# Optimization experiments

Hardware: AMD Instinct MI355X
Metric: run time of the kernel (lower is better)

The kernel has to match this reference:

```python
import jax, jax.numpy as jnp
import numpy as np
from jax import lax

H = 64            # hidden size
NUM_LAYERS = 3
EMBED_LEN = 128
B, T = 256, 2048


def _lstm_layer(x, Wih, Whh, bih, bhh):
    """x: [B, T, in]; returns full hidden sequence [B, T, H].
    PyTorch gate order: i, f, g, o."""
    Bn = x.shape[0]
    b = bih + bhh  # [4H]
    # Precompute input contribution for all timesteps: [T, B, 4H]
    xg = jnp.einsum('bti,gi->tbg', x, Wih) + b
    h0 = jnp.zeros((Bn, H), x.dtype)
    c0 = jnp.zeros((Bn, H), x.dtype)

    def step(carry, xg_t):
        h, c = carry
        gates = xg_t + h @ Whh.T  # [B, 4H]
        i, f, g, o = jnp.split(gates, 4, axis=-1)
        i = jax.nn.sigmoid(i)
        f = jax.nn.sigmoid(f)
        g = jnp.tanh(g)
        o = jax.nn.sigmoid(o)
        c = f * c + i * g
        h = o * jnp.tanh(c)
        return (h, c), h

    (_, _), hs = lax.scan(step, (h0, c0), xg)  # hs: [T, B, H]
    return jnp.swapaxes(hs, 0, 1)              # [B, T, H]


def setup_inputs() -> dict:
    key = jax.random.key(0)
    ks = jax.random.split(key, 20)
    k = 1.0 / np.sqrt(H)  # PyTorch default init bound

    def u(kk, shape):
        return jax.random.uniform(kk, shape, jnp.float32, -k, k)

    inp = {"x": jax.random.normal(ks[0], (B, 1, T), jnp.float32)}
    in_sizes = [1, H, H]
    idx = 1
    for l in range(NUM_LAYERS):
        inp[f"Wih{l}"] = u(ks[idx], (4 * H, in_sizes[l])); idx += 1
        inp[f"Whh{l}"] = u(ks[idx], (4 * H, H)); idx += 1
        inp[f"bih{l}"] = u(ks[idx], (4 * H,)); idx += 1
        inp[f"bhh{l}"] = u(ks[idx], (4 * H,)); idx += 1
    inp["fcW"] = u(ks[idx], (EMBED_LEN, H)); idx += 1
    inp["fcb"] = u(ks[idx], (EMBED_LEN,))
    return inp


def reference(x, Wih0, Whh0, bih0, bhh0,
              Wih1, Whh1, bih1, bhh1,
              Wih2, Whh2, bih2, bhh2,
              fcW, fcb):
    # forward: transpose [B,1,T] -> [B,T,1]
    h = jnp.swapaxes(x, 1, 2)
    h = _lstm_layer(h, Wih0, Whh0, bih0, bhh0)
    h = _lstm_layer(h, Wih1, Whh1, bih1, bhh1)
    h = _lstm_layer(h, Wih2, Whh2, bih2, bhh2)
    last = h[:, -1, :]              # [B, H]
    return last @ fcW.T + fcb       # [B, EMBED_LEN]
```

## Files before the change

kernel.cpp:

```cpp
#include <hip/hip_runtime.h>

#define T_LEN 2048
#define HID 64
#define EMB 128
#define WD 8
#define NWIN (T_LEN / WD)
#define NPH (NWIN + 4)
#define PPAD (HID + 4)

typedef _Float16 half2_t __attribute__((ext_vector_type(2)));
typedef _Float16 half4 __attribute__((ext_vector_type(4)));
typedef _Float16 half8 __attribute__((ext_vector_type(8)));
typedef float f32x4 __attribute__((ext_vector_type(4)));
typedef unsigned uint4v __attribute__((ext_vector_type(4)));

#if __has_builtin(__builtin_amdgcn_exp2f)
#define EXP2F(x) __builtin_amdgcn_exp2f(x)
#else
#define EXP2F(x) exp2f(x)
#endif
#if __has_builtin(__builtin_amdgcn_rcpf)
#define RCPF(x) __builtin_amdgcn_rcpf(x)
#else
#define RCPF(x) (1.0f / (x))
#endif

#define LOG2E 1.4426950408889634f

__device__ __forceinline__ float fdot2(unsigned a, unsigned b, float c) {
    return __builtin_amdgcn_fdot2(__builtin_bit_cast(half2_t, a),
                                  __builtin_bit_cast(half2_t, b), c, false);
}

__device__ __forceinline__ float dotrow(const uint4v* w, const uint4v* g, float init) {
    float a0 = init, a1 = 0.f, a2 = 0.f, a3 = 0.f;
    #pragma unroll
    for (int q = 0; q < 8; ++q) {
        a0 = fdot2(w[q][0], g[q][0], a0);
        a1 = fdot2(w[q][1], g[q][1], a1);
        a2 = fdot2(w[q][2], g[q][2], a2);
        a3 = fdot2(w[q][3], g[q][3], a3);
    }
    return (a0 + a1) + (a2 + a3);
}

__device__ __forceinline__ uint4v pack8(float4 a, float4 b, float s) {
    half2_t h0{(_Float16)(a.x * s), (_Float16)(a.y * s)};
    half2_t h1{(_Float16)(a.z * s), (_Float16)(a.w * s)};
    half2_t h2{(_Float16)(b.x * s), (_Float16)(b.y * s)};
    half2_t h3{(_Float16)(b.z * s), (_Float16)(b.w * s)};
    uint4v q;
    q[0] = __builtin_bit_cast(unsigned, h0);
    q[1] = __builtin_bit_cast(unsigned, h1);
    q[2] = __builtin_bit_cast(unsigned, h2);
    q[3] = __builtin_bit_cast(unsigned, h3);
    return q;
}

__device__ __forceinline__ void cvt8(const float* __restrict__ Wp, float s, uint4v* dst) {
    const float4* p = reinterpret_cast<const float4*>(Wp);
    #pragma unroll
    for (int k = 0; k < 8; ++k) dst[k] = pack8(p[2 * k], p[2 * k + 1], s);
}

__global__ __launch_bounds__(512)
__attribute__((amdgpu_waves_per_eu(2, 2)))
void lstm3_fused(
    const float* __restrict__ x,
    const float* __restrict__ Wih0, const float* __restrict__ Whh0,
    const float* __restrict__ bih0, const float* __restrict__ bhh0,
    const float* __restrict__ Wih1, const float* __restrict__ Whh1,
    const float* __restrict__ bih1, const float* __restrict__ bhh1,
    const float* __restrict__ Wih2, const float* __restrict__ Whh2,
    const float* __restrict__ bih2, const float* __restrict__ bhh2,
    const float* __restrict__ fcW,  const float* __restrict__ fcb,
    float* __restrict__ out)
{
    const int b   = blockIdx.x;
    const int tid = threadIdx.x;
    const int wv  = tid >> 6;
    const int L   = tid & 63;

    __shared__ __align__(16) _Float16 h0ring[16][HID];
    __shared__ __align__(16) _Float16 h1ring[16][HID];
    __shared__ __align__(16) _Float16 h2ring[2][HID];
    __shared__ __align__(16) float p1buf[2][WD][4][PPAD];
    __shared__ __align__(16) float p2buf[2][WD][4][PPAD];
    __shared__ __align__(16) float xs[T_LEN];

    {
        const float4* xg4 = reinterpret_cast<const float4*>(x + b * T_LEN);
        reinterpret_cast<float4*>(xs)[tid] = xg4[tid];
        reinterpret_cast<unsigned*>(h0ring)[tid] = 0u;
        reinterpret_cast<unsigned*>(h1ring)[tid] = 0u;
        if (tid < 64) reinterpret_cast<unsigned*>(h2ring)[tid] = 0u;
    }

    const float sI = -LOG2E, sF = -LOG2E, sG = -2.f * LOG2E, sO = -LOG2E;
    const float scl[4] = {sI, sF, sG, sO};

    uint4v w[4][8];
    float bias4[4] = {0.f, 0.f, 0.f, 0.f};
    float wx4[4]   = {0.f, 0.f, 0.f, 0.f};

    if (wv < 3) {
        const float* Wh = (wv == 0) ? Whh0 : (wv == 1) ? Whh1 : Whh2;
        const float* bi = (wv == 0) ? bih0 : (wv == 1) ? bih1 : bih2;
        const float* bh = (wv == 0) ? bhh0 : (wv == 1) ? bhh1 : bhh2;
        #pragma unroll
        for (int c = 0; c < 4; ++c) {
            cvt8(Wh + (c * 64 + L) * 64, scl[c], w[c]);
            bias4[c] = (bi[c * 64 + L] + bh[c * 64 + L]) * scl[c];
        }
        if (wv == 0) {
            #pragma unroll
            for (int c = 0; c < 4; ++c) wx4[c] = Wih0[c * 64 + L] * scl[c];
        }
    } else if (wv == 3 || wv == 7) {
        const float* Wsrc = (wv == 3) ? Wih1 : Wih2;
        const int g4 = (L >> 4) * 4;
        const int mr = L & 15;
        #pragma unroll
        for (int t = 0; t < 16; ++t) {
            const float s = scl[t >> 2];
            const float* rowp = Wsrc + (t * 16 + mr) * 64;
            #pragma unroll
            for (int kf = 0; kf < 2; ++kf) {
                float4 lo = *reinterpret_cast<const float4*>(rowp + kf * 32 + g4);
                float4 hi = *reinterpret_cast<const float4*>(rowp + kf * 32 + 16 + g4);
                half8 a = {(_Float16)(lo.x * s), (_Float16)(lo.y * s),
                           (_Float16)(lo.z * s), (_Float16)(lo.w * s),
                           (_Float16)(hi.x * s), (_Float16)(hi.y * s),
                           (_Float16)(hi.z * s), (_Float16)(hi.w * s)};
                const int idx = t * 2 + kf;
                w[idx >> 3][idx & 7] = __builtin_bit_cast(uint4v, a);
            }
        }
    }

    float cst = 0.f;
    __syncthreads();

    for (int ph = 0; ph < NPH; ++ph) {
        const int par = ph & 1;

        if (wv == 0) {
            if (ph < NWIN) {
                _Float16* cur = &h0ring[par * 8][0];
                const _Float16* prv = &h0ring[(par ^ 1) * 8][0];
                const int tb = ph * WD;
                #pragma unroll
                for (int j = 0; j < WD; ++j) {
                    const uint4v* hp = reinterpret_cast<const uint4v*>(
                        (j == 0) ? (prv + 7 * HID) : (cur + (j - 1) * HID));
                    uint4v g[8];
                    #pragma unroll
                    for (int k = 0; k < 8; ++k) g[k] = hp[k];
                    float xv = xs[tb + j];
                    float d0 = dotrow(w[0], g, fmaf(wx4[0], xv, bias4[0]));
                    float d1 = dotrow(w[1], g, fmaf(wx4[1], xv, bias4[1]));
                    float d2 = dotrow(w[2], g, fmaf(wx4[2], xv, bias4[2]));
                    float d3 = dotrow(w[3], g, fmaf(wx4[3], xv, bias4[3]));
                    float ai = RCPF(1.f + EXP2F(d0));
                    float af = RCPF(1.f + EXP2F(d1));
                    float ag = fmaf(2.f, RCPF(1.f + EXP2F(d2)), -1.f);
                    float ao = RCPF(1.f + EXP2F(d3));
                    cst = fmaf(af, cst, ai * ag);
                    float tc = fmaf(2.f, RCPF(1.f + EXP2F(-2.f * LOG2E * cst)), -1.f);
                    cur[j * HID + L] = (_Float16)(ao * tc);
                }
            }
        } else if (wv == 1) {
            if (ph >= 2 && ph < NWIN + 2) {
                _Float16* cur = &h1ring[par * 8][0];
                const _Float16* prv = &h1ring[(par ^ 1) * 8][0];
                const float (*pb)[4][PPAD] = p1buf[par];
                #pragma unroll
                for (int j = 0; j < WD; ++j) {
                    const uint4v* hp = reinterpret_cast<const uint4v*>(
                        (j == 0) ? (prv + 7 * HID) : (cur + (j - 1) * HID));
                    uint4v g[8];
                    #pragma unroll
                    for (int k = 0; k < 8; ++k) g[k] = hp[k];
                    float d0 = dotrow(w[0], g, bias4[0] + pb[j][0][L]);
                    float d1 = dotrow(w[1], g, bias4[1] + pb[j][1][L]);
                    float d2 = dotrow(w[2], g, bias4[2] + pb[j][2][L]);
                    float d3 = dotrow(w[3], g, bias4[3] + pb[j][3][L]);
                    float ai = RCPF(1.f + EXP2F(d0));
                    float af = RCPF(1.f + EXP2F(d1));
                    float ag = fmaf(2.f, RCPF(1.f + EXP2F(d2)), -1.f);
                    float ao = RCPF(1.f + EXP2F(d3));
                    cst = fmaf(af, cst, ai * ag);
                    float tc = fmaf(2.f, RCPF(1.f + EXP2F(-2.f * LOG2E * cst)), -1.f);
                    cur[j * HID + L] = (_Float16)(ao * tc);
                }
            }
        } else if (wv == 2) {
            if (ph >= 4) {
                const float (*pb)[4][PPAD] = p2buf[par];
                #pragma unroll
                for (int j = 0; j < WD; ++j) {
                    const uint4v* hp = reinterpret_cast<const uint4v*>(
                        &h2ring[(j & 1) ^ 1][0]);
                    uint4v g[8];
                    #pragma unroll
                    for (int k = 0; k < 8; ++k) g[k] = hp[k];
                    float d0 = dotrow(w[0], g, bias4[0] + pb[j][0][L]);
                    float d1 = dotrow(w[1], g, bias4[1] + pb[j][1][L]);
                    float d2 = dotrow(w[2], g, bias4[2] + pb[j][2][L]);
                    float d3 = dotrow(w[3], g, bias4[3] + pb[j][3][L]);
                    float ai = RCPF(1.f + EXP2F(d0));
                    float af = RCPF(1.f + EXP2F(d1));
                    float ag = fmaf(2.f, RCPF(1.f + EXP2F(d2)), -1.f);
                    float ao = RCPF(1.f + EXP2F(d3));
                    cst = fmaf(af, cst, ai * ag);
                    float tc = fmaf(2.f, RCPF(1.f + EXP2F(-2.f * LOG2E * cst)), -1.f);
                    h2ring[j & 1][L] = (_Float16)(ao * tc);
                }
            }
        } else if (wv == 3 || wv == 7) {
            const bool act = (wv == 3) ? (ph >= 1 && ph < NWIN + 1)
                                       : (ph >= 3 && ph < NWIN + 3);
            if (act) {
                const _Float16 (*ring)[HID] = (wv == 3) ? h0ring : h1ring;
                float (*po)[4][PPAD] = ((wv == 3) ? p1buf : p2buf)[par ^ 1];
                const int jj = L & 7;
                const int g4 = (L >> 4) * 4;
                const _Float16* rb = &ring[(par ^ 1) * 8 + jj][0];
                half4 b00 = *reinterpret_cast<const half4*>(rb + g4);
                half4 b01 = *reinterpret_cast<const half4*>(rb + 16 + g4);
                half4 b10 = *reinterpret_cast<const half4*>(rb + 32 + g4);
                half4 b11 = *reinterpret_cast<const half4*>(rb + 48 + g4);
                half8 B0 = __builtin_shufflevector(b00, b01, 0, 1, 2, 3, 4, 5, 6, 7);
                half8 B1 = __builtin_shufflevector(b10, b11, 0, 1, 2, 3, 4, 5, 6, 7);
                f32x4 acc[16];
                #pragma unroll
                for (int t = 0; t < 16; ++t) {
                    const int i0 = t * 2, i1 = t * 2 + 1;
                    f32x4 z = {0.f, 0.f, 0.f, 0.f};
                    acc[t] = __builtin_amdgcn_mfma_f32_16x16x32_f16(
                        __builtin_bit_cast(half8, w[i0 >> 3][i0 & 7]), B0, z, 0, 0, 0);
                    acc[t] = __builtin_amdgcn_mfma_f32_16x16x32_f16(
                        __builtin_bit_cast(half8, w[i1 >> 3][i1 & 7]), B1, acc[t], 0, 0, 0);
                }
                if ((L & 15) < 8) {
                    #pragma unroll
                    for (int t = 0; t < 16; ++t) {
                        *reinterpret_cast<f32x4*>(
                            &po[jj][t >> 2][(t & 3) * 16 + g4]) = acc[t];
                    }
                }
            }
        }

        __syncthreads();
    }

    if (tid < EMB) {
        float acc = fcb[tid];
        const _Float16* hf = &h2ring[1][0];
        const float4* W4 = reinterpret_cast<const float4*>(fcW + tid * HID);
        #pragma unroll
        for (int k = 0; k < 16; ++k) {
            float4 wv4 = W4[k];
            acc = fmaf(wv4.x, (float)hf[4 * k + 0], acc);
            acc = fmaf(wv4.y, (float)hf[4 * k + 1], acc);
            acc = fmaf(wv4.z, (float)hf[4 * k + 2], acc);
            acc = fmaf(wv4.w, (float)hf[4 * k + 3], acc);
        }
        out[b * EMB + tid] = acc;
    }
}

extern "C" void kernel_launch(void* const* d_in, const int* in_sizes, int n_in,
                              void* d_out, int out_size, void* d_ws, size_t ws_size,
                              hipStream_t stream) {
    const float* x    = (const float*)d_in[0];
    const float* Wih0 = (const float*)d_in[1];
    const float* Whh0 = (const float*)d_in[2];
    const float* bih0 = (const float*)d_in[3];
    const float* bhh0 = (const float*)d_in[4];
    const float* Wih1 = (const float*)d_in[5];
    const float* Whh1 = (const float*)d_in[6];
    const float* bih1 = (const float*)d_in[7];
    const float* bhh1 = (const float*)d_in[8];
    const float* Wih2 = (const float*)d_in[9];
    const float* Whh2 = (const float*)d_in[10];
    const float* bih2 = (const float*)d_in[11];
    const float* bhh2 = (const float*)d_in[12];
    const float* fcW  = (const float*)d_in[13];
    const float* fcb  = (const float*)d_in[14];
    float* out = (float*)d_out;

    lstm3_fused<<<dim3(256), dim3(512), 0, stream>>>(
        x, Wih0, Whh0, bih0, bhh0,
        Wih1, Whh1, bih1, bhh1,
        Wih2, Whh2, bih2, bhh2,
        fcW, fcb, out);
}
```

Before: 1.021 ms.

## Pipeline LSTM layers across blocks with MFMA batching over 32 samples

Replaces the one-block-per-sample kernel, where waves handled the three layers of a single sequence, with 24 blocks: 8 sample groups by 3 layers. Each block runs 32 samples at once and computes the recurrent gates with MFMA over the batch dimension. Hidden states stream between layer blocks through a global-memory ring buffer, coordinated by acquire/release flag spinning. This trades a large per-sample serial dot-product cost for batched tensor-core work. The risks are that only 24 CUs are used, inter-block flag latency sits on every step, and the design relies on all 24 blocks being co-resident to avoid deadlock.

```diff
diff --git a/kernel.cpp b/kernel.cpp
--- a/kernel.cpp
+++ b/kernel.cpp
@@ -3,16 +3,14 @@
 #define T_LEN 2048
 #define HID 64
 #define EMB 128
-#define WD 8
-#define NWIN (T_LEN / WD)
-#define NPH (NWIN + 4)
-#define PPAD (HID + 4)
-
-typedef _Float16 half2_t __attribute__((ext_vector_type(2)));
-typedef _Float16 half4 __attribute__((ext_vector_type(4)));
-typedef _Float16 half8 __attribute__((ext_vector_type(8)));
+#define NGRP 8
+#define SPG 32
+#define RSLOT 64
+#define HPAD 68
+
+typedef _Float16 half4v __attribute__((ext_vector_type(4)));
+typedef _Float16 half8v __attribute__((ext_vector_type(8)));
 typedef float f32x4 __attribute__((ext_vector_type(4)));
-typedef unsigned uint4v __attribute__((ext_vector_type(4)));
 
 #if __has_builtin(__builtin_amdgcn_exp2f)
 #define EXP2F(x) __builtin_amdgcn_exp2f(x)
@@ -27,45 +25,25 @@
 
 #define LOG2E 1.4426950408889634f
 
-__device__ __forceinline__ float fdot2(unsigned a, unsigned b, float c) {
-    return __builtin_amdgcn_fdot2(__builtin_bit_cast(half2_t, a),
-                                  __builtin_bit_cast(half2_t, b), c, false);
-}
-
-__device__ __forceinline__ float dotrow(const uint4v* w, const uint4v* g, float init) {
-    float a0 = init, a1 = 0.f, a2 = 0.f, a3 = 0.f;
-    #pragma unroll
-    for (int q = 0; q < 8; ++q) {
-        a0 = fdot2(w[q][0], g[q][0], a0);
-        a1 = fdot2(w[q][1], g[q][1], a1);
-        a2 = fdot2(w[q][2], g[q][2], a2);
-        a3 = fdot2(w[q][3], g[q][3], a3);
-    }
-    return (a0 + a1) + (a2 + a3);
-}
-
-__device__ __forceinline__ uint4v pack8(float4 a, float4 b, float s) {
-    half2_t h0{(_Float16)(a.x * s), (_Float16)(a.y * s)};
-    half2_t h1{(_Float16)(a.z * s), (_Float16)(a.w * s)};
-    half2_t h2{(_Float16)(b.x * s), (_Float16)(b.y * s)};
-    half2_t h3{(_Float16)(b.z * s), (_Float16)(b.w * s)};
-    uint4v q;
-    q[0] = __builtin_bit_cast(unsigned, h0);
-    q[1] = __builtin_bit_cast(unsigned, h1);
-    q[2] = __builtin_bit_cast(unsigned, h2);
-    q[3] = __builtin_bit_cast(unsigned, h3);
-    return q;
-}
-
-__device__ __forceinline__ void cvt8(const float* __restrict__ Wp, float s, uint4v* dst) {
-    const float4* p = reinterpret_cast<const float4*>(Wp);
-    #pragma unroll
-    for (int k = 0; k < 8; ++k) dst[k] = pack8(p[2 * k], p[2 * k + 1], s);
+__device__ __forceinline__ half8v ldA(const float* __restrict__ rowp, int kbase,
+                                      int g4, float s) {
+    float4 lo = *reinterpret_cast<const float4*>(rowp + kbase + g4);
+    float4 hi = *reinterpret_cast<const float4*>(rowp + kbase + 16 + g4);
+    half8v a = {(_Float16)(lo.x * s), (_Float16)(lo.y * s),
+                (_Float16)(lo.z * s), (_Float16)(lo.w * s),
+                (_Float16)(hi.x * s), (_Float16)(hi.y * s),
+                (_Float16)(hi.z * s), (_Float16)(hi.w * s)};
+    return a;
+}
+
+__device__ __forceinline__ half8v ldB(const _Float16* base, int kbase, int g4) {
+    half4v lo = *reinterpret_cast<const half4v*>(base + kbase + g4);
+    half4v hi = *reinterpret_cast<const half4v*>(base + kbase + 16 + g4);
+    return __builtin_shufflevector(lo, hi, 0, 1, 2, 3, 4, 5, 6, 7);
 }
 
 __global__ __launch_bounds__(512)
-__attribute__((amdgpu_waves_per_eu(2, 2)))
-void lstm3_fused(
+void lstm3_pipe(
     const float* __restrict__ x,
     const float* __restrict__ Wih0, const float* __restrict__ Whh0,
     const float* __restrict__ bih0, const float* __restrict__ bhh0,
@@ -74,201 +52,185 @@
     const float* __restrict__ Wih2, const float* __restrict__ Whh2,
     const float* __restrict__ bih2, const float* __restrict__ bhh2,
     const float* __restrict__ fcW,  const float* __restrict__ fcb,
-    float* __restrict__ out)
+    float* __restrict__ out, char* __restrict__ ws)
 {
-    const int b   = blockIdx.x;
+    const int bid = blockIdx.x;
+    const int lay = bid >> 3;
+    const int grp = bid & 7;
     const int tid = threadIdx.x;
     const int wv  = tid >> 6;
+    const int qd  = wv >> 2;
+    const int q   = wv & 3;
     const int L   = tid & 63;
-
-    __shared__ __align__(16) _Float16 h0ring[16][HID];
-    __shared__ __align__(16) _Float16 h1ring[16][HID];
-    __shared__ __align__(16) _Float16 h2ring[2][HID];
-    __shared__ __align__(16) float p1buf[2][WD][4][PPAD];
-    __shared__ __align__(16) float p2buf[2][WD][4][PPAD];
-    __shared__ __align__(16) float xs[T_LEN];
-
-    {
-        const float4* xg4 = reinterpret_cast<const float4*>(x + b * T_LEN);
-        reinterpret_cast<float4*>(xs)[tid] = xg4[tid];
-        reinterpret_cast<unsigned*>(h0ring)[tid] = 0u;
-        reinterpret_cast<unsigned*>(h1ring)[tid] = 0u;
-        if (tid < 64) reinterpret_cast<unsigned*>(h2ring)[tid] = 0u;
-    }
+    const int mr  = L & 15;
+    const int lg  = L >> 4;
+    const int g4  = 4 * lg;
+    const int sl  = 16 * qd + mr;
+    const int sample = SPG * grp + sl;
+
+    __shared__ __align__(16) _Float16 hbuf[2][SPG][HPAD];
+
+    int* flags = (int*)ws;
+    int* prod0 = flags + grp;
+    int* cons0 = flags + 8 + grp;
+    int* prod1 = flags + 16 + grp;
+    int* cons1 = flags + 24 + grp;
+    int* pf_in  = (lay == 2) ? prod1 : prod0;
+    int* cf_pub = (lay == 2) ? cons1 : cons0;
+    int* pf_pub = (lay == 0) ? prod0 : prod1;
+    int* cf_thr = (lay == 0) ? cons0 : cons1;
+
+    const size_t STREAM_ELEMS = (size_t)NGRP * RSLOT * SPG * HID;
+    _Float16* st0 = (_Float16*)(ws + 1024);
+    _Float16* st1 = st0 + STREAM_ELEMS;
+    const _Float16* stin = (lay == 2) ? st1 : st0;
+    _Float16*      stout = (lay == 0) ? st0 : st1;
+
+    for (int i = tid; i < 2176; i += 512)
+        reinterpret_cast<unsigned*>(hbuf)[i] = 0u;
 
     const float sI = -LOG2E, sF = -LOG2E, sG = -2.f * LOG2E, sO = -LOG2E;
     const float scl[4] = {sI, sF, sG, sO};
-
-    uint4v w[4][8];
-    float bias4[4] = {0.f, 0.f, 0.f, 0.f};
-    float wx4[4]   = {0.f, 0.f, 0.f, 0.f};
-
-    if (wv < 3) {
-        const float* Wh = (wv == 0) ? Whh0 : (wv == 1) ? Whh1 : Whh2;
-        const float* bi = (wv == 0) ? bih0 : (wv == 1) ? bih1 : bih2;
-        const float* bh = (wv == 0) ? bhh0 : (wv == 1) ? bhh1 : bhh2;
+    const float* Whh = (lay == 0) ? Whh0 : (lay == 1) ? Whh1 : Whh2;
+    const float* Wih = (lay == 0) ? Wih0 : (lay == 1) ? Wih1 : Wih2;
+    const float* bi  = (lay == 0) ? bih0 : (lay == 1) ? bih1 : bih2;
+    const float* bh  = (lay == 0) ? bhh0 : (lay == 1) ? bhh1 : bhh2;
+
+    half8v a4[4][4];
+    f32x4 biasv[4], w0x[4];
+    #pragma unroll
+    for (int g = 0; g < 4; ++g) {
+        const int rowA = 64 * g + 16 * q + mr;
+        const float* rp = Whh + rowA * 64;
+        a4[g][0] = ldA(rp, 0, g4, scl[g]);
+        a4[g][1] = ldA(rp, 32, g4, scl[g]);
+        if (lay > 0) {
+            const float* rp2 = Wih + rowA * 64;
+            a4[g][2] = ldA(rp2, 0, g4, scl[g]);
+            a4[g][3] = ldA(rp2, 32, g4, scl[g]);
+        }
+        const int rowD = 64 * g + 16 * q + 4 * lg;
+        f32x4 bv, wvv;
         #pragma unroll
-        for (int c = 0; c < 4; ++c) {
-            cvt8(Wh + (c * 64 + L) * 64, scl[c], w[c]);
-            bias4[c] = (bi[c * 64 + L] + bh[c * 64 + L]) * scl[c];
-        }
-        if (wv == 0) {
+        for (int r = 0; r < 4; ++r) bv[r] = (bi[rowD + r] + bh[rowD + r]) * scl[g];
+        biasv[g] = bv;
+        if (lay == 0) {
             #pragma unroll
-            for (int c = 0; c < 4; ++c) wx4[c] = Wih0[c * 64 + L] * scl[c];
-        }
-    } else if (wv == 3 || wv == 7) {
-        const float* Wsrc = (wv == 3) ? Wih1 : Wih2;
-        const int g4 = (L >> 4) * 4;
-        const int mr = L & 15;
+            for (int r = 0; r < 4; ++r) wvv[r] = Wih[rowD + r] * scl[g];
+            w0x[g] = wvv;
+        }
+    }
+
+    float cs[4] = {0.f, 0.f, 0.f, 0.f};
+    float xv_c = 0.f;
+    half8v B2c{}, B3c{};
+
+    __syncthreads();
+
+    if (lay == 0) {
+        xv_c = x[(size_t)sample * T_LEN];
+    } else {
+        while (__hip_atomic_load(pf_in, __ATOMIC_ACQUIRE, __HIP_MEMORY_SCOPE_AGENT) < 12)
+            __builtin_amdgcn_s_sleep(2);
+        const _Float16* sp = stin + (((size_t)grp * RSLOT + 0) * SPG + sl) * HID;
+        B2c = ldB(sp, 0, g4);
+        B3c = ldB(sp, 32, g4);
+    }
+
+    for (int t = 0; t < T_LEN; ++t) {
+        if ((t & 7) == 0) {
+            if (lay > 0) {
+                int need = t + 12; if (need > T_LEN) need = T_LEN;
+                while (__hip_atomic_load(pf_in, __ATOMIC_ACQUIRE, __HIP_MEMORY_SCOPE_AGENT) < need)
+                    __builtin_amdgcn_s_sleep(2);
+            }
+            if (lay < 2) {
+                while (__hip_atomic_load(cf_thr, __ATOMIC_RELAXED, __HIP_MEMORY_SCOPE_AGENT)
+                       + (RSLOT - 16) < t)
+                    __builtin_amdgcn_s_sleep(2);
+            }
+        }
+
+        float xv = xv_c;
+        half8v B2 = B2c, B3 = B3c;
+        const int tn = (t < T_LEN - 1) ? t + 1 : T_LEN - 1;
+        if (lay == 0) {
+            xv_c = x[(size_t)sample * T_LEN + tn];
+        } else {
+            const _Float16* sp = stin +
+                (((size_t)grp * RSLOT + (tn & (RSLOT - 1))) * SPG + sl) * HID;
+            B2c = ldB(sp, 0, g4);
+            B3c = ldB(sp, 32, g4);
+        }
+
+        const _Float16* hb = &hbuf[(t & 1) ^ 1][sl][0];
+        half8v B0 = ldB(hb, 0, g4);
+        half8v B1 = ldB(hb, 32, g4);
+
+        f32x4 acc[4];
         #pragma unroll
-        for (int t = 0; t < 16; ++t) {
-            const float s = scl[t >> 2];
-            const float* rowp = Wsrc + (t * 16 + mr) * 64;
+        for (int g = 0; g < 4; ++g) {
+            f32x4 cin = biasv[g];
+            if (lay == 0) {
+                #pragma unroll
+                for (int r = 0; r < 4; ++r) cin[r] = fmaf(w0x[g][r], xv, cin[r]);
+            }
+            f32x4 a = __builtin_amdgcn_mfma_f32_16x16x32_f16(a4[g][0], B0, cin, 0, 0, 0);
+            a = __builtin_amdgcn_mfma_f32_16x16x32_f16(a4[g][1], B1, a, 0, 0, 0);
+            if (lay > 0) {
+                a = __builtin_amdgcn_mfma_f32_16x16x32_f16(a4[g][2], B2, a, 0, 0, 0);
+                a = __builtin_amdgcn_mfma_f32_16x16x32_f16(a4[g][3], B3, a, 0, 0, 0);
+            }
+            acc[g] = a;
+        }
+
+        float hv[4];
+        #pragma unroll
+        for (int r = 0; r < 4; ++r) {
+            float d0 = acc[0][r], d1 = acc[1][r], d2 = acc[2][r], d3 = acc[3][r];
+            float ai = RCPF(1.f + EXP2F(d0));
+            float af = RCPF(1.f + EXP2F(d1));
+            float ag = fmaf(2.f, RCPF(1.f + EXP2F(d2)), -1.f);
+            float ao = RCPF(1.f + EXP2F(d3));
+            cs[r] = fmaf(af, cs[r], ai * ag);
+            float tc = fmaf(2.f, RCPF(1.f + EXP2F(-2.f * LOG2E * cs[r])), -1.f);
+            hv[r] = ao * tc;
+        }
+        half4v h4 = {(_Float16)hv[0], (_Float16)hv[1], (_Float16)hv[2], (_Float16)hv[3]};
+
+        *reinterpret_cast<half4v*>(&hbuf[t & 1][sl][16 * q + g4]) = h4;
+        if (lay < 2) {
+            _Float16* op = stout +
+                (((size_t)grp * RSLOT + (t & (RSLOT - 1))) * SPG + sl) * HID + 16 * q + g4;
+            *reinterpret_cast<half4v*>(op) = h4;
+        }
+
+        __syncthreads();
+
+        if (tid == 0) {
+            if (lay < 2 && (t & 3) == 3)
+                __hip_atomic_store(pf_pub, t + 1, __ATOMIC_RELEASE, __HIP_MEMORY_SCOPE_AGENT);
+            if (lay > 0 && (t & 7) == 7)
+                __hip_atomic_store(cf_pub, t + 1, __ATOMIC_RELAXED, __HIP_MEMORY_SCOPE_AGENT);
+        }
+    }
+
+    if (lay == 2) {
+        for (int idx = tid; idx < SPG * EMB; idx += 512) {
+            const int sm = idx >> 7, e = idx & 127;
+            float acc2 = fcb[e];
+            const _Float16* hf = &hbuf[1][sm][0];
+            const float4* W4 = reinterpret_cast<const float4*>(fcW + e * HID);
             #pragma unroll
-            for (int kf = 0; kf < 2; ++kf) {
-                float4 lo = *reinterpret_cast<const float4*>(rowp + kf * 32 + g4);
-                float4 hi = *reinterpret_cast<const float4*>(rowp + kf * 32 + 16 + g4);
-                half8 a = {(_Float16)(lo.x * s), (_Float16)(lo.y * s),
-                           (_Float16)(lo.z * s), (_Float16)(lo.w * s),
-                           (_Float16)(hi.x * s), (_Float16)(hi.y * s),
-                           (_Float16)(hi.z * s), (_Float16)(hi.w * s)};
-                const int idx = t * 2 + kf;
-                w[idx >> 3][idx & 7] = __builtin_bit_cast(uint4v, a);
-            }
-        }
-    }
-
-    float cst = 0.f;
-    __syncthreads();
-
-    for (int ph = 0; ph < NPH; ++ph) {
-        const int par = ph & 1;
-
-        if (wv == 0) {
-            if (ph < NWIN) {
-                _Float16* cur = &h0ring[par * 8][0];
-                const _Float16* prv = &h0ring[(par ^ 1) * 8][0];
-                const int tb = ph * WD;
-                #pragma unroll
-                for (int j = 0; j < WD; ++j) {
-                    const uint4v* hp = reinterpret_cast<const uint4v*>(
-                        (j == 0) ? (prv + 7 * HID) : (cur + (j - 1) * HID));
-                    uint4v g[8];
-                    #pragma unroll
-                    for (int k = 0; k < 8; ++k) g[k] = hp[k];
-                    float xv = xs[tb + j];
-                    float d0 = dotrow(w[0], g, fmaf(wx4[0], xv, bias4[0]));
-                    float d1 = dotrow(w[1], g, fmaf(wx4[1], xv, bias4[1]));
-                    float d2 = dotrow(w[2], g, fmaf(wx4[2], xv, bias4[2]));
-                    float d3 = dotrow(w[3], g, fmaf(wx4[3], xv, bias4[3]));
-                    float ai = RCPF(1.f + EXP2F(d0));
-                    float af = RCPF(1.f + EXP2F(d1));
-                    float ag = fmaf(2.f, RCPF(1.f + EXP2F(d2)), -1.f);
-                    float ao = RCPF(1.f + EXP2F(d3));
-                    cst = fmaf(af, cst, ai * ag);
-                    float tc = fmaf(2.f, RCPF(1.f + EXP2F(-2.f * LOG2E * cst)), -1.f);
-                    cur[j * HID + L] = (_Float16)(ao * tc);
-                }
-            }
-        } else if (wv == 1) {
-            if (ph >= 2 && ph < NWIN + 2) {
-                _Float16* cur = &h1ring[par * 8][0];
-                const _Float16* prv = &h1ring[(par ^ 1) * 8][0];
-                const float (*pb)[4][PPAD] = p1buf[par];
-                #pragma unroll
-                for (int j = 0; j < WD; ++j) {
-                    const uint4v* hp = reinterpret_cast<const uint4v*>(
-                        (j == 0) ? (prv + 7 * HID) : (cur + (j - 1) * HID));
-                    uint4v g[8];
-                    #pragma unroll
-                    for (int k = 0; k < 8; ++k) g[k] = hp[k];
-                    float d0 = dotrow(w[0], g, bias4[0] + pb[j][0][L]);
-                    float d1 = dotrow(w[1], g, bias4[1] + pb[j][1][L]);
-                    float d2 = dotrow(w[2], g, bias4[2] + pb[j][2][L]);
-                    float d3 = dotrow(w[3], g, bias4[3] + pb[j][3][L]);
-                    float ai = RCPF(1.f + EXP2F(d0));
-                    float af = RCPF(1.f + EXP2F(d1));
-                    float ag = fmaf(2.f, RCPF(1.f + EXP2F(d2)), -1.f);
-                    float ao = RCPF(1.f + EXP2F(d3));
-                    cst = fmaf(af, cst, ai * ag);
-                    float tc = fmaf(2.f, RCPF(1.f + EXP2F(-2.f * LOG2E * cst)), -1.f);
-                    cur[j * HID + L] = (_Float16)(ao * tc);
-                }
-            }
-        } else if (wv == 2) {
-            if (ph >= 4) {
-                const float (*pb)[4][PPAD] = p2buf[par];
-                #pragma unroll
-                for (int j = 0; j < WD; ++j) {
-                    const uint4v* hp = reinterpret_cast<const uint4v*>(
-                        &h2ring[(j & 1) ^ 1][0]);
-                    uint4v g[8];
-                    #pragma unroll
-                    for (int k = 0; k < 8; ++k) g[k] = hp[k];
-                    float d0 = dotrow(w[0], g, bias4[0] + pb[j][0][L]);
-                    float d1 = dotrow(w[1], g, bias4[1] + pb[j][1][L]);
-                    float d2 = dotrow(w[2], g, bias4[2] + pb[j][2][L]);
-                    float d3 = dotrow(w[3], g, bias4[3] + pb[j][3][L]);
-                    float ai = RCPF(1.f + EXP2F(d0));
-                    float af = RCPF(1.f + EXP2F(d1));
-                    float ag = fmaf(2.f, RCPF(1.f + EXP2F(d2)), -1.f);
-                    float ao = RCPF(1.f + EXP2F(d3));
-                    cst = fmaf(af, cst, ai * ag);
-                    float tc = fmaf(2.f, RCPF(1.f + EXP2F(-2.f * LOG2E * cst)), -1.f);
-                    h2ring[j & 1][L] = (_Float16)(ao * tc);
-                }
-            }
-        } else if (wv == 3 || wv == 7) {
-            const bool act = (wv == 3) ? (ph >= 1 && ph < NWIN + 1)
-                                       : (ph >= 3 && ph < NWIN + 3);
-            if (act) {
-                const _Float16 (*ring)[HID] = (wv == 3) ? h0ring : h1ring;
-                float (*po)[4][PPAD] = ((wv == 3) ? p1buf : p2buf)[par ^ 1];
-                const int jj = L & 7;
-                const int g4 = (L >> 4) * 4;
-                const _Float16* rb = &ring[(par ^ 1) * 8 + jj][0];
-                half4 b00 = *reinterpret_cast<const half4*>(rb + g4);
-                half4 b01 = *reinterpret_cast<const half4*>(rb + 16 + g4);
-                half4 b10 = *reinterpret_cast<const half4*>(rb + 32 + g4);
-                half4 b11 = *reinterpret_cast<const half4*>(rb + 48 + g4);
-                half8 B0 = __builtin_shufflevector(b00, b01, 0, 1, 2, 3, 4, 5, 6, 7);
-                half8 B1 = __builtin_shufflevector(b10, b11, 0, 1, 2, 3, 4, 5, 6, 7);
-                f32x4 acc[16];
-                #pragma unroll
-                for (int t = 0; t < 16; ++t) {
-                    const int i0 = t * 2, i1 = t * 2 + 1;
-                    f32x4 z = {0.f, 0.f, 0.f, 0.f};
-                    acc[t] = __builtin_amdgcn_mfma_f32_16x16x32_f16(
-                        __builtin_bit_cast(half8, w[i0 >> 3][i0 & 7]), B0, z, 0, 0, 0);
-                    acc[t] = __builtin_amdgcn_mfma_f32_16x16x32_f16(
-                        __builtin_bit_cast(half8, w[i1 >> 3][i1 & 7]), B1, acc[t], 0, 0, 0);
-                }
-                if ((L & 15) < 8) {
-                    #pragma unroll
-                    for (int t = 0; t < 16; ++t) {
-                        *reinterpret_cast<f32x4*>(
-                            &po[jj][t >> 2][(t & 3) * 16 + g4]) = acc[t];
-                    }
-                }
-            }
-        }
-
-        __syncthreads();
-    }
-
-    if (tid < EMB) {
-        float acc = fcb[tid];
-        const _Float16* hf = &h2ring[1][0];
-        const float4* W4 = reinterpret_cast<const float4*>(fcW + tid * HID);
-        #pragma unroll
-        for (int k = 0; k < 16; ++k) {
-            float4 wv4 = W4[k];
-            acc = fmaf(wv4.x, (float)hf[4 * k + 0], acc);
-            acc = fmaf(wv4.y, (float)hf[4 * k + 1], acc);
-            acc = fmaf(wv4.z, (float)hf[4 * k + 2], acc);
-            acc = fmaf(wv4.w, (float)hf[4 * k + 3], acc);
-        }
-        out[b * EMB + tid] = acc;
+            for (int k = 0; k < 16; ++k) {
+                float4 w4 = W4[k];
+                acc2 = fmaf(w4.x, (float)hf[4 * k + 0], acc2);
+                acc2 = fmaf(w4.y, (float)hf[4 * k + 1], acc2);
+                acc2 = fmaf(w4.z, (float)hf[4 * k + 2], acc2);
+                acc2 = fmaf(w4.w, (float)hf[4 * k + 3], acc2);
+            }
+            out[(size_t)(SPG * grp + sm) * EMB + e] = acc2;
+        }
     }
 }
 
@@ -292,9 +254,10 @@
     const float* fcb  = (const float*)d_in[14];
     float* out = (float*)d_out;
 
-    lstm3_fused<<<dim3(256), dim3(512), 0, stream>>>(
+    hipMemsetAsync(d_ws, 0, 1024, stream);
+    lstm3_pipe<<<dim3(24), dim3(512), 0, stream>>>(
         x, Wih0, Whh0, bih0, bhh0,
         Wih1, Whh1, bih1, bhh1,
         Wih2, Whh2, bih2, bhh2,
-        fcW, fcb, out);
-}
+        fcW, fcb, out, (char*)d_ws);
+}
```

Result: slower. 2.987 ms (+192.5%).
